# Performance work log

Measured on AMD Instinct MI355X. Metric: run time of the kernel, lower is better.

The kernel has to match this reference:

```python
import jax, jax.numpy as jnp
import numpy as np

H = 8  # num attention heads (hard-coded in the torch module)
NEG_SLOPE = 0.2  # DGL GATConv default leaky_relu slope


def setup_inputs() -> dict:
    key = jax.random.key(0)
    ks = jax.random.split(key, 7)
    B, L, F = 32, 4096, 128
    s = 0.02
    loc = jax.random.normal(ks[0], (B, L, F), jnp.float32)
    W_src = jax.random.normal(ks[1], (H * F, F), jnp.float32) * s
    W_dst = jax.random.normal(ks[2], (H * F, F), jnp.float32) * s
    attn_l = jax.random.normal(ks[3], (H, F), jnp.float32) * s
    attn_r = jax.random.normal(ks[4], (H, F), jnp.float32) * s
    W_res = jax.random.normal(ks[5], (H * F, F), jnp.float32) * s
    bias = jnp.zeros((H * F,), jnp.float32)
    return {"loc": loc, "W_src": W_src, "W_dst": W_dst, "attn_l": attn_l,
            "attn_r": attn_r, "W_res": W_res, "bias": bias}


def reference(loc, W_src, W_dst, attn_l, attn_r, W_res, bias):
    B, L, F = loc.shape
    E = L - 1
    # chain graph: edge i connects src node i (type A) -> dst node i (type B)
    u = jnp.arange(E)
    v = jnp.arange(E)
    u_feat = loc[:, :E]   # (B,E,F) src node features
    v_feat = loc[:, 1:]   # (B,E,F) dst node features
    Ws = W_src.reshape(H, F, F)
    Wd = W_dst.reshape(H, F, F)
    Wr = W_res.reshape(H, F, F)
    h_src = jnp.einsum('bne,hoe->bnho', u_feat, Ws)  # (B,E,H,F)
    h_dst = jnp.einsum('bne,hoe->bnho', v_feat, Wd)  # (B,E,H,F)
    el = jnp.einsum('bnho,ho->bnh', h_src, attn_l)   # (B,E,H)
    er = jnp.einsum('bnho,ho->bnh', h_dst, attn_r)   # (B,E,H)
    e = jax.nn.leaky_relu(el[:, u] + er[:, v], NEG_SLOPE)  # per-edge score (B,E,H)
    # edge softmax over incoming edges of each dst node (segments on axis 0)
    et = jnp.moveaxis(e, 1, 0)                        # (E,B,H)
    m = jax.ops.segment_max(et, v, num_segments=E)
    ee = jnp.exp(et - m[v])
    denom = jax.ops.segment_sum(ee, v, num_segments=E)
    alpha = ee / denom[v]                             # (E,B,H)
    # weighted scatter-aggregate of src features to dst nodes
    msg = jnp.moveaxis(h_src[:, u], 1, 0) * alpha[..., None]      # (E,B,H,F)
    rst = jnp.moveaxis(jax.ops.segment_sum(msg, v, num_segments=E), 0, 1)  # (B,E,H,F)
    # residual projection of dst features + bias (DGL GATConv residual=True)
    resval = jnp.einsum('bne,hoe->bnho', v_feat, Wr)
    rst = rst + resval + bias.reshape(H, F)
    res = rst.mean(axis=2)                            # mean over heads -> (B,E,F)
    return jnp.concatenate([loc[:, :1], res], axis=1)  # prepend origin -> (B,L,F)
```

## Files before the change

kernel.cpp:

```cpp
#include <hip/hip_runtime.h>

namespace {

constexpr int F = 128;
constexpr int L = 4096;

using short8 = __attribute__((ext_vector_type(8))) short;
using f32x16 = __attribute__((ext_vector_type(16))) float;
using u32x4  = __attribute__((ext_vector_type(4))) unsigned int;

__device__ inline unsigned short f2bf(float x) {
    unsigned u = __builtin_bit_cast(unsigned, x);
    unsigned r = (u + 0x7fffu + ((u >> 16) & 1u)) >> 16;
    return (unsigned short)r;
}

__device__ inline unsigned pack2(float lo, float hi) {
    return (unsigned)f2bf(lo) | ((unsigned)f2bf(hi) << 16);
}

__global__ void prep(const float* __restrict__ Wsrc,
                     const float* __restrict__ Wres,
                     const float* __restrict__ bias,
                     unsigned short* __restrict__ Wf,
                     float* __restrict__ bbar)
{
    int idx = blockIdx.x * 256 + threadIdx.x;
    if (idx < 2 * F * F) {
        int j  = idx & 7;
        int r2 = idx >> 3;
        int l  = r2 & 63;
        int c  = r2 >> 6;
        int cg = c >> 4;
        int S  = c & 15;
        int h  = l >> 5;
        int k  = S * 16 + h * 8 + j;
        int n  = (cg << 5) + (l & 31);
        int e  = k & (F - 1);
        const float* W = (k < F) ? Wsrc : Wres;
        float sum = 0.f;
#pragma unroll
        for (int hh = 0; hh < 8; ++hh) sum += W[(hh * F + n) * F + e];
        Wf[idx] = f2bf(sum * 0.125f);
    }
    if (idx < F) {
        float s = 0.f;
#pragma unroll
        for (int hh = 0; hh < 8; ++hh) s += bias[hh * F + idx];
        bbar[idx] = s * 0.125f;
    }
}

__global__ __launch_bounds__(256, 2)
void gat_cg(const float* __restrict__ loc,
            const unsigned short* __restrict__ Wf,
            const float* __restrict__ bbar,
            float* __restrict__ out)
{
    __shared__ unsigned short As[65 * 128];

    const int t    = threadIdx.x;
    const int lane = t & 63;
    const int cg   = t >> 6;
    const int l31  = lane & 31;
    const int h    = lane >> 5;
    const long rowbase = (long)blockIdx.x * 64;

    u32x4 wu[16];
#pragma unroll
    for (int s = 0; s < 16; ++s)
        wu[s] = *(const u32x4*)(Wf + (((cg * 16 + s) * 64 + lane) << 3));

    const float bb = bbar[cg * 32 + l31];

#pragma unroll
    for (int i = 0; i < 5; ++i) {
        int c = i * 256 + t;
        if (i < 4 || c < 1040) {
            int r  = c >> 4;
            int sl = c & 15;
            long g = rowbase - 1 + r;
            if (g < 0) g = 0;
            const float* src = loc + g * F + sl * 8;
            float4 v0 = *(const float4*)(src);
            float4 v1 = *(const float4*)(src + 4);
            u32x4 pk;
            pk[0] = pack2(v0.x, v0.y);
            pk[1] = pack2(v0.z, v0.w);
            pk[2] = pack2(v1.x, v1.y);
            pk[3] = pack2(v1.z, v1.w);
            *(u32x4*)((char*)As + r * 256 + ((sl * 16) ^ ((r & 15) << 4))) = pk;
        }
    }
    __syncthreads();

    f32x16 acc0, acc1;
#pragma unroll
    for (int i = 0; i < 16; ++i) { acc0[i] = 0.f; acc1[i] = 0.f; }

#pragma unroll
    for (int s = 0; s < 16; ++s) {
        const int d   = (s < 8) ? 0 : 1;
        const int off = (s & 7) * 32 + h * 16;
        const int r0  = l31 + d;
        const int r1  = 32 + l31 + d;
        short8 x0 = *(const short8*)((const char*)As + r0 * 256 + (off ^ ((r0 & 15) << 4)));
        short8 x1 = *(const short8*)((const char*)As + r1 * 256 + (off ^ ((r1 & 15) << 4)));
        short8 w  = __builtin_bit_cast(short8, wu[s]);
        acc0 = __builtin_amdgcn_mfma_f32_32x32x16_bf16(x0, w, acc0, 0, 0, 0);
        acc1 = __builtin_amdgcn_mfma_f32_32x32x16_bf16(x1, w, acc1, 0, 0, 0);
    }

    const int col = cg * 32 + l31;
#pragma unroll
    for (int reg = 0; reg < 16; ++reg) {
        const int rl = (reg & 3) + 8 * (reg >> 2) + 4 * h;
        {
            long grow = rowbase + rl;
            float v = acc0[reg] + bb;
            if ((grow & (L - 1)) == 0) v = loc[grow * F + col];
            out[grow * F + col] = v;
        }
        {
            long grow = rowbase + 32 + rl;
            out[grow * F + col] = acc1[reg] + bb;
        }
    }
}

}

extern "C" void kernel_launch(void* const* d_in, const int* in_sizes, int n_in,
                              void* d_out, int out_size, void* d_ws, size_t ws_size,
                              hipStream_t stream) {
    const float* loc  = (const float*)d_in[0];
    const float* Wsrc = (const float*)d_in[1];
    const float* Wres = (const float*)d_in[5];
    const float* bias = (const float*)d_in[6];

    unsigned short* Wf   = (unsigned short*)d_ws;
    float*          bbar = (float*)((char*)d_ws + 2 * F * F * 2);
    float*          outp = (float*)d_out;

    prep<<<128, 256, 0, stream>>>(Wsrc, Wres, bias, Wf, bbar);

    gat_cg<<<2048, 256, 0, stream>>>(loc, Wf, bbar, outp);
}
```

Baseline: 31.90 us.

## Process four row tiles per block with double-buffered LDS prefetch

```diff
diff --git a/kernel.cpp b/kernel.cpp
--- a/kernel.cpp
+++ b/kernel.cpp
@@ -2,8 +2,10 @@
 
 namespace {
 
-constexpr int F = 128;
-constexpr int L = 4096;
+constexpr int F   = 128;
+constexpr int L   = 4096;
+constexpr int TPB = 4;
+constexpr int NB  = 2048 / TPB;
 
 using short8 = __attribute__((ext_vector_type(8))) short;
 using f32x16 = __attribute__((ext_vector_type(16))) float;
@@ -51,20 +53,61 @@
     }
 }
 
+#define ISSUE_LOADS(BASE)                                                  \
+    {                                                                      \
+        _Pragma("unroll")                                                  \
+        for (int i = 0; i < 4; ++i) {                                      \
+            int c = i * 256 + t;                                           \
+            long g = (BASE) - 1 + (c >> 4);                                \
+            if (g < 0) g = 0;                                              \
+            const float* src = loc + g * F + (c & 15) * 8;                 \
+            sv[i * 2]     = *(const float4*)(src);                         \
+            sv[i * 2 + 1] = *(const float4*)(src + 4);                     \
+        }                                                                  \
+        if (t < 16) {                                                      \
+            const float* src = loc + ((BASE) + 63) * F + t * 8;            \
+            hv0 = *(const float4*)(src);                                   \
+            hv1 = *(const float4*)(src + 4);                               \
+        }                                                                  \
+    }
+
+#define PACK_WRITE(BUF)                                                    \
+    {                                                                      \
+        _Pragma("unroll")                                                  \
+        for (int i = 0; i < 4; ++i) {                                      \
+            int c = i * 256 + t;                                           \
+            int r = c >> 4, sl = c & 15;                                   \
+            u32x4 pk;                                                      \
+            pk[0] = pack2(sv[i * 2].x,     sv[i * 2].y);                   \
+            pk[1] = pack2(sv[i * 2].z,     sv[i * 2].w);                   \
+            pk[2] = pack2(sv[i * 2 + 1].x, sv[i * 2 + 1].y);               \
+            pk[3] = pack2(sv[i * 2 + 1].z, sv[i * 2 + 1].w);               \
+            *(u32x4*)((char*)As[BUF] + r * 256 + ((sl * 16) ^ ((r & 15) << 4))) = pk; \
+        }                                                                  \
+        if (t < 16) {                                                      \
+            u32x4 pk;                                                      \
+            pk[0] = pack2(hv0.x, hv0.y);                                   \
+            pk[1] = pack2(hv0.z, hv0.w);                                   \
+            pk[2] = pack2(hv1.x, hv1.y);                                   \
+            pk[3] = pack2(hv1.z, hv1.w);                                   \
+            *(u32x4*)((char*)As[BUF] + 64 * 256 + (t * 16)) = pk;          \
+        }                                                                  \
+    }
+
 __global__ __launch_bounds__(256, 2)
-void gat_cg(const float* __restrict__ loc,
-            const unsigned short* __restrict__ Wf,
-            const float* __restrict__ bbar,
-            float* __restrict__ out)
+void gat_pipe(const float* __restrict__ loc,
+              const unsigned short* __restrict__ Wf,
+              const float* __restrict__ bbar,
+              float* __restrict__ out)
 {
-    __shared__ unsigned short As[65 * 128];
+    __shared__ unsigned short As[2][65 * 128];
 
     const int t    = threadIdx.x;
     const int lane = t & 63;
     const int cg   = t >> 6;
     const int l31  = lane & 31;
     const int h    = lane >> 5;
-    const long rowbase = (long)blockIdx.x * 64;
+    const long row0 = (long)blockIdx.x * (64 * TPB);
 
     u32x4 wu[16];
 #pragma unroll
@@ -73,57 +116,58 @@
 
     const float bb = bbar[cg * 32 + l31];
 
-#pragma unroll
-    for (int i = 0; i < 5; ++i) {
-        int c = i * 256 + t;
-        if (i < 4 || c < 1040) {
-            int r  = c >> 4;
-            int sl = c & 15;
-            long g = rowbase - 1 + r;
-            if (g < 0) g = 0;
-            const float* src = loc + g * F + sl * 8;
-            float4 v0 = *(const float4*)(src);
-            float4 v1 = *(const float4*)(src + 4);
-            u32x4 pk;
-            pk[0] = pack2(v0.x, v0.y);
-            pk[1] = pack2(v0.z, v0.w);
-            pk[2] = pack2(v1.x, v1.y);
-            pk[3] = pack2(v1.z, v1.w);
-            *(u32x4*)((char*)As + r * 256 + ((sl * 16) ^ ((r & 15) << 4))) = pk;
-        }
-    }
+    float4 sv[8];
+    float4 hv0, hv1;
+
+    ISSUE_LOADS(row0)
+    asm volatile("" ::: "memory");
+    PACK_WRITE(0)
     __syncthreads();
 
-    f32x16 acc0, acc1;
 #pragma unroll
-    for (int i = 0; i < 16; ++i) { acc0[i] = 0.f; acc1[i] = 0.f; }
+    for (int it = 0; it < TPB; ++it) {
+        const long tbase = row0 + (long)it * 64;
+        const int  buf   = it & 1;
+
+        if (it + 1 < TPB) ISSUE_LOADS(tbase + 64)
+        asm volatile("" ::: "memory");
+
+        f32x16 acc0, acc1;
+#pragma unroll
+        for (int i = 0; i < 16; ++i) { acc0[i] = 0.f; acc1[i] = 0.f; }
 
 #pragma unroll
-    for (int s = 0; s < 16; ++s) {
-        const int d   = (s < 8) ? 0 : 1;
-        const int off = (s & 7) * 32 + h * 16;
-        const int r0  = l31 + d;
-        const int r1  = 32 + l31 + d;
-        short8 x0 = *(const short8*)((const char*)As + r0 * 256 + (off ^ ((r0 & 15) << 4)));
-        short8 x1 = *(const short8*)((const char*)As + r1 * 256 + (off ^ ((r1 & 15) << 4)));
-        short8 w  = __builtin_bit_cast(short8, wu[s]);
-        acc0 = __builtin_amdgcn_mfma_f32_32x32x16_bf16(x0, w, acc0, 0, 0, 0);
-        acc1 = __builtin_amdgcn_mfma_f32_32x32x16_bf16(x1, w, acc1, 0, 0, 0);
-    }
+        for (int s = 0; s < 16; ++s) {
+            const int d   = (s < 8) ? 0 : 1;
+            const int off = (s & 7) * 32 + h * 16;
+            const int r0  = l31 + d;
+            const int r1  = 32 + l31 + d;
+            short8 x0 = *(const short8*)((const char*)As[buf] + r0 * 256 + (off ^ ((r0 & 15) << 4)));
+            short8 x1 = *(const short8*)((const char*)As[buf] + r1 * 256 + (off ^ ((r1 & 15) << 4)));
+            short8 w  = __builtin_bit_cast(short8, wu[s]);
+            acc0 = __builtin_amdgcn_mfma_f32_32x32x16_bf16(x0, w, acc0, 0, 0, 0);
+            acc1 = __builtin_amdgcn_mfma_f32_32x32x16_bf16(x1, w, acc1, 0, 0, 0);
+        }
 
-    const int col = cg * 32 + l31;
+        const int col = cg * 32 + l31;
 #pragma unroll
-    for (int reg = 0; reg < 16; ++reg) {
-        const int rl = (reg & 3) + 8 * (reg >> 2) + 4 * h;
-        {
-            long grow = rowbase + rl;
-            float v = acc0[reg] + bb;
-            if ((grow & (L - 1)) == 0) v = loc[grow * F + col];
-            out[grow * F + col] = v;
+        for (int reg = 0; reg < 16; ++reg) {
+            const int rl = (reg & 3) + 8 * (reg >> 2) + 4 * h;
+            {
+                long grow = tbase + rl;
+                float v = acc0[reg] + bb;
+                if ((grow & (L - 1)) == 0) v = loc[grow * F + col];
+                out[grow * F + col] = v;
+            }
+            {
+                long grow = tbase + 32 + rl;
+                out[grow * F + col] = acc1[reg] + bb;
+            }
         }
-        {
-            long grow = rowbase + 32 + rl;
-            out[grow * F + col] = acc1[reg] + bb;
+
+        if (it + 1 < TPB) {
+            PACK_WRITE(buf ^ 1)
+            __syncthreads();
         }
     }
 }
@@ -144,5 +188,5 @@
 
     prep<<<128, 256, 0, stream>>>(Wsrc, Wres, bias, Wf, bbar);
 
-    gat_cg<<<2048, 256, 0, stream>>>(loc, Wf, bbar, outp);
+    gat_pipe<<<NB, 256, 0, stream>>>(loc, Wf, bbar, outp);
 }
```

New measurement: 32.09 us. About the same (+0.6%).
